# Kernel optimization log

Hardware: AMD Instinct MI355X
Metric: run time of the kernel (lower is better)

Reference implementation:

```python
import jax, jax.numpy as jnp
import numpy as np

B, CIN, H, W = 4, 1024, 64, 64
PLANES = 256
K = 3
DIL = 2
PAD = DIL * (K - 1) // 2  # = 2
EPS = 1e-5


def setup_inputs() -> dict:
    key = jax.random.key(0)
    ks = jax.random.split(key, 16)
    d = {}
    d['x'] = jax.random.normal(ks[0], (B, CIN, H, W), dtype=jnp.float32)
    # conv1: 1x1, inplanes->planes, no bias
    d['w1'] = jax.random.normal(ks[1], (PLANES, CIN), dtype=jnp.float32) * 0.02
    d['gamma1'] = jnp.ones((PLANES,), jnp.float32)
    d['beta1'] = jnp.zeros((PLANES,), jnp.float32)
    d['mean1'] = jax.random.normal(ks[2], (PLANES,), dtype=jnp.float32) * 0.1
    d['var1'] = jax.random.uniform(ks[3], (PLANES,), minval=0.5, maxval=1.5, dtype=jnp.float32)
    # deform_offset: 3x3 conv planes->18, with bias
    d['woff'] = jax.random.normal(ks[4], (18, PLANES, K, K), dtype=jnp.float32) * 0.01
    d['boff'] = jnp.zeros((18,), jnp.float32)
    # conv2 (deformable): 3x3 planes->planes, with bias
    d['w2'] = jax.random.normal(ks[5], (PLANES, PLANES, K, K), dtype=jnp.float32) * 0.02
    d['bconv2'] = jnp.zeros((PLANES,), jnp.float32)
    d['gamma2'] = jnp.ones((PLANES,), jnp.float32)
    d['beta2'] = jnp.zeros((PLANES,), jnp.float32)
    d['mean2'] = jax.random.normal(ks[6], (PLANES,), dtype=jnp.float32) * 0.1
    d['var2'] = jax.random.uniform(ks[7], (PLANES,), minval=0.5, maxval=1.5, dtype=jnp.float32)
    # conv3: 1x1 planes->planes*4, no bias
    d['w3'] = jax.random.normal(ks[8], (PLANES * 4, PLANES), dtype=jnp.float32) * 0.02
    d['gamma3'] = jnp.ones((PLANES * 4,), jnp.float32)
    d['beta3'] = jnp.zeros((PLANES * 4,), jnp.float32)
    d['mean3'] = jax.random.normal(ks[9], (PLANES * 4,), dtype=jnp.float32) * 0.1
    d['var3'] = jax.random.uniform(ks[10], (PLANES * 4,), minval=0.5, maxval=1.5, dtype=jnp.float32)
    return d


def _bn(x, gamma, beta, mean, var):
    # inference-mode BatchNorm over channel dim (NCHW)
    inv = jax.lax.rsqrt(var + EPS)
    return (x - mean[:, None, None]) * (inv * gamma)[:, None, None] + beta[:, None, None]


def _deform_conv(x, offset, w, b):
    # x: [B,C,H,W]; offset: [B,18,H,W] ordered (dy,dx) per kernel tap; w: [O,C,3,3]
    Bn, C, Hh, Ww = x.shape
    off = offset.reshape(Bn, K * K, 2, Hh, Ww)
    off_y, off_x = off[:, :, 0], off[:, :, 1]          # [B,9,H,W]
    kk = jnp.arange(K * K)
    base_y = (kk // K) * DIL - PAD                      # [9]
    base_x = (kk % K) * DIL - PAD
    ys = jnp.arange(Hh, dtype=x.dtype)
    xs = jnp.arange(Ww, dtype=x.dtype)
    py = base_y.astype(x.dtype)[None, :, None, None] + ys[None, None, :, None] + off_y
    px = base_x.astype(x.dtype)[None, :, None, None] + xs[None, None, None, :] + off_x

    def sample_one(img, py1, px1):
        # img [C,H,W]; py1/px1 [9,H,W] -> [C,9,H,W] bilinear with zero padding
        y0 = jnp.floor(py1)
        x0 = jnp.floor(px1)
        wy = py1 - y0
        wx = px1 - x0

        def gather(yc, xc):
            yi = yc.astype(jnp.int32)
            xi = xc.astype(jnp.int32)
            valid = ((yi >= 0) & (yi < Hh) & (xi >= 0) & (xi < Ww)).astype(img.dtype)
            yi = jnp.clip(yi, 0, Hh - 1)
            xi = jnp.clip(xi, 0, Ww - 1)
            return img[:, yi, xi] * valid[None]

        v00 = gather(y0, x0)
        v01 = gather(y0, x0 + 1)
        v10 = gather(y0 + 1, x0)
        v11 = gather(y0 + 1, x0 + 1)
        return (v00 * ((1 - wy) * (1 - wx))[None] + v01 * ((1 - wy) * wx)[None]
                + v10 * (wy * (1 - wx))[None] + v11 * (wy * wx)[None])

    sampled = jax.vmap(sample_one)(x, py, px)           # [B,C,9,H,W]
    out = jnp.einsum('bckhw,ock->bohw', sampled, w.reshape(w.shape[0], C, K * K))
    return out + b[None, :, None, None]


def reference(x, w1, gamma1, beta1, mean1, var1, woff, boff, w2, bconv2,
              gamma2, beta2, mean2, var2, w3, gamma3, beta3, mean3, var3):
    residual = x
    out = jnp.einsum('bchw,oc->bohw', x, w1)            # conv1 1x1
    out = jax.nn.relu(_bn(out, gamma1, beta1, mean1, var1))
    offset = jax.lax.conv_general_dilated(
        out, woff, window_strides=(1, 1), padding=((PAD, PAD), (PAD, PAD)),
        rhs_dilation=(DIL, DIL), dimension_numbers=('NCHW', 'OIHW', 'NCHW'))
    offset = offset + boff[None, :, None, None]
    out = _deform_conv(out, offset, w2, bconv2)
    out = jax.nn.relu(_bn(out, gamma2, beta2, mean2, var2))
    out = jnp.einsum('bchw,oc->bohw', out, w3)          # conv3 1x1
    out = _bn(out, gamma3, beta3, mean3, var3)
    return jax.nn.relu(out + residual)
```

## Files before the change

kernel.cpp:

```cpp
#include <hip/hip_runtime.h>

#define EPS_BN 1e-5f

typedef __bf16 bf16x8 __attribute__((ext_vector_type(8)));
typedef float f32x4 __attribute__((ext_vector_type(4)));

__device__ __forceinline__ unsigned short f2bf(float f) {
  union { float f; unsigned u; } v; v.f = f;
  unsigned r = v.u + 0x7fffu + ((v.u >> 16) & 1u);
  return (unsigned short)(r >> 16);
}
__device__ __forceinline__ float bf2f(unsigned short h) {
  union { unsigned u; float f; } v; v.u = ((unsigned)h) << 16;
  return v.f;
}

__global__ void cvt_bf16(const float* __restrict__ in, unsigned short* __restrict__ out, int n) {
  int i = blockIdx.x * 256 + threadIdx.x;
  if (i < n) out[i] = f2bf(in[i]);
}

__global__ void zero16(uint4* __restrict__ p, int n16) {
  int i = blockIdx.x * 256 + threadIdx.x;
  if (i < n16) p[i] = uint4{0, 0, 0, 0};
}

__global__ void reorder_w2(const float* __restrict__ w2, unsigned short* __restrict__ w2r) {
  int i = blockIdx.x * 256 + threadIdx.x;
  int o = i / 2304, r = i % 2304;
  int kk = r / 256, c = r % 256;
  w2r[i] = f2bf(w2[(size_t)o * 2304 + c * 9 + kk]);
}

__global__ void reorder_woff(const float* __restrict__ woff, unsigned short* __restrict__ wob) {
  int i = blockIdx.x * 256 + threadIdx.x;
  if (i >= 32 * 2304) return;
  int o = i / 2304, r = i % 2304;
  int kk = r / 256, c = r % 256;
  wob[i] = (o < 18) ? f2bf(woff[(size_t)o * 2304 + c * 9 + kk]) : (unsigned short)0;
}

__global__ __launch_bounds__(256) void transpose_x(const float* __restrict__ x,
                                                   unsigned short* __restrict__ xT) {
  __shared__ float t[32][33];
  int b = blockIdx.z;
  int p0 = blockIdx.x * 32, c0 = blockIdx.y * 32;
  int tx = threadIdx.x & 31, ty = threadIdx.x >> 5;
  const float* xb = x + (size_t)b * 1024 * 4096;
#pragma unroll
  for (int j = 0; j < 4; ++j) {
    int c = c0 + ty + j * 8;
    t[ty + j * 8][tx] = xb[(size_t)c * 4096 + p0 + tx];
  }
  __syncthreads();
  unsigned short* xTb = xT + (size_t)b * 4096 * 1024;
#pragma unroll
  for (int j = 0; j < 4; ++j) {
    int p = p0 + ty + j * 8;
    xTb[(size_t)p * 1024 + c0 + tx] = f2bf(t[tx][ty + j * 8]);
  }
}

template <int EPI>
__global__ __launch_bounds__(256) void gemm_bt(
    const unsigned short* __restrict__ A, const unsigned short* __restrict__ Bm,
    void* __restrict__ outp, unsigned short* __restrict__ out2,
    const float* __restrict__ gamma, const float* __restrict__ beta,
    const float* __restrict__ mean, const float* __restrict__ var,
    const float* __restrict__ bias, const float* __restrict__ resid,
    int M, int N, int K, long bStrideB, long bStrideOut) {
  __shared__ unsigned short sA[128 * 32];
  __shared__ unsigned short sB[128 * 32];
  int tid = threadIdx.x, lane = tid & 63, wv = tid >> 6;
  int z = blockIdx.z;
  const unsigned short* Bz = Bm + (size_t)z * bStrideB;
  int m0 = blockIdx.y * 128, n0 = blockIdx.x * 128;
  f32x4 acc[4][4] = {};
  int rowA = tid >> 2;
  int kcol = (tid & 3) * 8;
  int wm = wv & 1, wn = wv >> 1;
  int lane15 = lane & 15, quad8 = (lane >> 4) * 8;

  for (int k0 = 0; k0 < K; k0 += 32) {
    __syncthreads();
#pragma unroll
    for (int r = 0; r < 2; ++r) {
      const unsigned short* gp = A + (size_t)(m0 + r * 64 + rowA) * K + k0 + kcol;
      __builtin_amdgcn_global_load_lds((const __attribute__((address_space(1))) void*)gp,
                                       (__attribute__((address_space(3))) void*)&sA[r * 2048 + wv * 512],
                                       16, 0, 0);
    }
#pragma unroll
    for (int r = 0; r < 2; ++r) {
      const unsigned short* gp = Bz + (size_t)(n0 + r * 64 + rowA) * K + k0 + kcol;
      __builtin_amdgcn_global_load_lds((const __attribute__((address_space(1))) void*)gp,
                                       (__attribute__((address_space(3))) void*)&sB[r * 2048 + wv * 512],
                                       16, 0, 0);
    }
    __syncthreads();
    bf16x8 afr[4], bfr[4];
#pragma unroll
    for (int mi = 0; mi < 4; ++mi)
      afr[mi] = *(const bf16x8*)&sA[(wm * 64 + mi * 16 + lane15) * 32 + quad8];
#pragma unroll
    for (int ni = 0; ni < 4; ++ni)
      bfr[ni] = *(const bf16x8*)&sB[(wn * 64 + ni * 16 + lane15) * 32 + quad8];
#pragma unroll
    for (int mi = 0; mi < 4; ++mi)
#pragma unroll
      for (int ni = 0; ni < 4; ++ni)
        acc[mi][ni] = __builtin_amdgcn_mfma_f32_16x16x32_bf16(afr[mi], bfr[ni], acc[mi][ni], 0, 0, 0);
  }

  if constexpr (EPI == 3) {
    float* outF = (float*)outp + (size_t)z * bStrideOut;
    const float* res = resid + (size_t)z * bStrideOut;
#pragma unroll
    for (int mi = 0; mi < 4; ++mi) {
#pragma unroll
      for (int ni = 0; ni < 4; ++ni) {
        int col = n0 + wn * 64 + ni * 16 + lane15;
#pragma unroll
        for (int reg = 0; reg < 4; ++reg) {
          int row = m0 + wm * 64 + mi * 16 + (lane >> 4) * 4 + reg;
          int ch = row;
          float inv = rsqrtf(var[ch] + EPS_BN) * gamma[ch];
          float v = (acc[mi][ni][reg] - mean[ch]) * inv + beta[ch];
          v += res[(size_t)row * N + col];
          outF[(size_t)row * N + col] = fmaxf(v, 0.f);
        }
      }
    }
  } else {
    unsigned short* outH = (unsigned short*)outp;
#pragma unroll
    for (int mi = 0; mi < 4; ++mi) {
#pragma unroll
      for (int ni = 0; ni < 4; ++ni) {
        int col = n0 + wn * 64 + ni * 16 + lane15;
        int ch = col;
        float inv = rsqrtf(var[ch] + EPS_BN) * gamma[ch];
        float mu = mean[ch], bt = beta[ch];
        float bi = (EPI == 2) ? bias[ch] : 0.f;
#pragma unroll
        for (int reg = 0; reg < 4; ++reg) {
          int row = m0 + wm * 64 + mi * 16 + (lane >> 4) * 4 + reg;
          float v = acc[mi][ni][reg] + bi;
          v = (v - mu) * inv + bt;
          unsigned short hv = f2bf(fmaxf(v, 0.f));
          outH[(size_t)row * N + col] = hv;
          if constexpr (EPI == 1) {
            int b = row >> 12, p = row & 4095;
            out2[(((size_t)(b * 68) + (p >> 6) + 2) * 68 + (p & 63) + 2) * 256 + col] = hv;
          }
        }
      }
    }
  }
}

__global__ __launch_bounds__(256) void off_gemm(const unsigned short* __restrict__ actP,
                                                const unsigned short* __restrict__ wob,
                                                const float* __restrict__ boff,
                                                float* __restrict__ offsP) {
  __shared__ unsigned short sA[64 * 64];
  __shared__ unsigned short sB[32 * 64];
  int tid = threadIdx.x, lane = tid & 63, wv = tid >> 6;
  int m0 = blockIdx.x * 64;
  int lane15 = lane & 15, quad8 = (lane >> 4) * 8;
  int rowA = tid >> 3;
  int kc = (tid & 7) * 8;

  const unsigned short* baseA[2];
#pragma unroll
  for (int r = 0; r < 2; ++r) {
    int row = m0 + r * 32 + rowA;
    int b = row >> 12, p = row & 4095;
    baseA[r] = actP + (((size_t)(b * 68) + (p >> 6) + 2) * 68 + (p & 63) + 2) * 256 + kc;
  }
  const unsigned short* baseB = wob + (size_t)rowA * 2304 + kc;

  f32x4 acc[2] = {};
  for (int kk = 0; kk < 9; ++kk) {
    int shift = ((kk / 3) * 2 - 2) * 68 + ((kk % 3) * 2 - 2);
#pragma unroll 1
    for (int c0 = 0; c0 < 256; c0 += 64) {
      __syncthreads();
#pragma unroll
      for (int r = 0; r < 2; ++r) {
        const unsigned short* gp = baseA[r] + (long)shift * 256 + c0;
        __builtin_amdgcn_global_load_lds((const __attribute__((address_space(1))) void*)gp,
                                         (__attribute__((address_space(3))) void*)&sA[r * 2048 + wv * 512],
                                         16, 0, 0);
      }
      {
        const unsigned short* gp = baseB + kk * 256 + c0;
        __builtin_amdgcn_global_load_lds((const __attribute__((address_space(1))) void*)gp,
                                         (__attribute__((address_space(3))) void*)&sB[wv * 512],
                                         16, 0, 0);
      }
      __syncthreads();
      bf16x8 afr[2], bfr[2][2];
#pragma unroll
      for (int kq = 0; kq < 2; ++kq) {
        afr[kq] = *(const bf16x8*)&sA[(wv * 16 + lane15) * 64 + kq * 32 + quad8];
#pragma unroll
        for (int ni = 0; ni < 2; ++ni)
          bfr[kq][ni] = *(const bf16x8*)&sB[(ni * 16 + lane15) * 64 + kq * 32 + quad8];
      }
#pragma unroll
      for (int kq = 0; kq < 2; ++kq)
#pragma unroll
        for (int ni = 0; ni < 2; ++ni)
          acc[ni] = __builtin_amdgcn_mfma_f32_16x16x32_bf16(afr[kq], bfr[kq][ni], acc[ni], 0, 0, 0);
    }
  }

#pragma unroll
  for (int ni = 0; ni < 2; ++ni) {
    int o = ni * 16 + lane15;
    if (o < 18) {
      float bo = boff[o];
#pragma unroll
      for (int reg = 0; reg < 4; ++reg) {
        int row = m0 + wv * 16 + (lane >> 4) * 4 + reg;
        offsP[(size_t)row * 18 + o] = acc[ni][reg] + bo;
      }
    }
  }
}

__global__ __launch_bounds__(256) void deform_sample(const unsigned short* __restrict__ act1T,
                                                     const float* __restrict__ offsP,
                                                     unsigned short* __restrict__ S) {
  int g = threadIdx.x >> 5, t = threadIdx.x & 31;
  int idx = blockIdx.x * 8 + g;
  int b = idx >> 12, p = idx & 4095;
  int h = p >> 6, w = p & 63;
  const unsigned short* actb = act1T + (size_t)b * 4096 * 256 + t * 8;
  unsigned short* Sp = S + (size_t)idx * 2304 + t * 8;
  float ov = (t < 18) ? offsP[(size_t)idx * 18 + t] : 0.f;
#pragma unroll
  for (int kk = 0; kk < 9; ++kk) {
    float offy = __shfl(ov, 2 * kk, 32);
    float offx = __shfl(ov, 2 * kk + 1, 32);
    float py = (float)(h + (kk / 3) * 2 - 2) + offy;
    float px = (float)(w + (kk % 3) * 2 - 2) + offx;
    float fy = floorf(py), fx = floorf(px);
    int y0 = (int)fy, x0 = (int)fx;
    float wy = py - fy, wx = px - fx;
    bool yv0 = (y0 >= 0 && y0 < 64), yv1 = (y0 >= -1 && y0 < 63);
    bool xv0 = (x0 >= 0 && x0 < 64), xv1 = (x0 >= -1 && x0 < 63);
    const unsigned short* cb = actb + (y0 * 64 + x0) * 256;
    uint4 q00{0,0,0,0}, q01{0,0,0,0}, q10{0,0,0,0}, q11{0,0,0,0};
    if (yv0 && xv0) q00 = *(const uint4*)(cb);
    if (yv0 && xv1) q01 = *(const uint4*)(cb + 256);
    if (yv1 && xv0) q10 = *(const uint4*)(cb + 64 * 256);
    if (yv1 && xv1) q11 = *(const uint4*)(cb + 64 * 256 + 256);
    float w00 = (1.f - wy) * (1.f - wx), w01 = (1.f - wy) * wx;
    float w10 = wy * (1.f - wx), w11 = wy * wx;
    unsigned u00[4] = {q00.x, q00.y, q00.z, q00.w};
    unsigned u01[4] = {q01.x, q01.y, q01.z, q01.w};
    unsigned u10[4] = {q10.x, q10.y, q10.z, q10.w};
    unsigned u11[4] = {q11.x, q11.y, q11.z, q11.w};
    unsigned out[4];
#pragma unroll
    for (int j = 0; j < 4; ++j) {
      float lo = bf2f((unsigned short)(u00[j] & 0xffffu)) * w00 +
                 bf2f((unsigned short)(u01[j] & 0xffffu)) * w01 +
                 bf2f((unsigned short)(u10[j] & 0xffffu)) * w10 +
                 bf2f((unsigned short)(u11[j] & 0xffffu)) * w11;
      float hi = bf2f((unsigned short)(u00[j] >> 16)) * w00 +
                 bf2f((unsigned short)(u01[j] >> 16)) * w01 +
                 bf2f((unsigned short)(u10[j] >> 16)) * w10 +
                 bf2f((unsigned short)(u11[j] >> 16)) * w11;
      out[j] = (unsigned)f2bf(lo) | ((unsigned)f2bf(hi) << 16);
    }
    *(uint4*)(Sp + kk * 256) = uint4{out[0], out[1], out[2], out[3]};
  }
}

extern "C" void kernel_launch(void* const* d_in, const int* in_sizes, int n_in,
                              void* d_out, int out_size, void* d_ws, size_t ws_size,
                              hipStream_t stream) {
  const float* x      = (const float*)d_in[0];
  const float* w1     = (const float*)d_in[1];
  const float* gamma1 = (const float*)d_in[2];
  const float* beta1  = (const float*)d_in[3];
  const float* mean1  = (const float*)d_in[4];
  const float* var1   = (const float*)d_in[5];
  const float* woff   = (const float*)d_in[6];
  const float* boff   = (const float*)d_in[7];
  const float* w2     = (const float*)d_in[8];
  const float* bconv2 = (const float*)d_in[9];
  const float* gamma2 = (const float*)d_in[10];
  const float* beta2  = (const float*)d_in[11];
  const float* mean2  = (const float*)d_in[12];
  const float* var2   = (const float*)d_in[13];
  const float* w3     = (const float*)d_in[14];
  const float* gamma3 = (const float*)d_in[15];
  const float* beta3  = (const float*)d_in[16];
  const float* mean3  = (const float*)d_in[17];
  const float* var3   = (const float*)d_in[18];

  char* ws = (char*)d_ws;
  unsigned short* xT    = (unsigned short*)(ws);
  unsigned short* act1T = (unsigned short*)(ws + 33554432);
  unsigned short* act2T = (unsigned short*)(ws + 41943040);
  unsigned short* S     = (unsigned short*)(ws + 50331648);
  float*          offs  = (float*)(ws + 125829120);
  unsigned short* w1b   = (unsigned short*)(ws + 127008768);
  unsigned short* w2r   = (unsigned short*)(ws + 127533056);
  unsigned short* w3b   = (unsigned short*)(ws + 128712704);
  unsigned short* act1P = S;
  unsigned short* wob   = xT;

  cvt_bf16<<<1024, 256, 0, stream>>>(w1, w1b, 262144);
  cvt_bf16<<<1024, 256, 0, stream>>>(w3, w3b, 262144);
  reorder_w2<<<2304, 256, 0, stream>>>(w2, w2r);
  zero16<<<2312, 256, 0, stream>>>((uint4*)act1P, 591872);
  transpose_x<<<dim3(128, 32, 4), 256, 0, stream>>>(x, xT);

  gemm_bt<1><<<dim3(2, 128, 1), 256, 0, stream>>>(xT, w1b, act1T, act1P, gamma1, beta1, mean1,
                                                  var1, nullptr, nullptr, 16384, 256, 1024, 0, 0);
  reorder_woff<<<288, 256, 0, stream>>>(woff, wob);
  off_gemm<<<256, 256, 0, stream>>>(act1P, wob, boff, offs);
  deform_sample<<<dim3(2048), 256, 0, stream>>>(act1T, offs, S);
  gemm_bt<2><<<dim3(2, 128, 1), 256, 0, stream>>>(S, w2r, act2T, nullptr, gamma2, beta2, mean2,
                                                  var2, bconv2, nullptr, 16384, 256, 2304, 0, 0);
  gemm_bt<3><<<dim3(32, 8, 4), 256, 0, stream>>>(w3b, act2T, d_out, nullptr, gamma3, beta3, mean3,
                                                 var3, nullptr, x, 1024, 4096, 256, 4096L * 256,
                                                 4194304L);
}
```

Baseline: 325.9 us.

## Split-K the conv1 and deformable GEMMs with a separate vectorized BN epilogue

The two M=16384,N=256 GEMMs ran only 256 blocks each. They now use split-K by two (512 blocks), writing fp32 partials that a new vectorized epilogue kernel sums before applying precomputed BN scale and shift, ReLU and bf16 packing, including the padded copy. This adds fp32 partial-sum traffic of about 32MB written and read per GEMM, plus extra launches. In exchange it gets more parallelism and coalesced 16-byte epilogue stores in place of scattered 2-byte stores.

```diff
diff --git a/kernel.cpp b/kernel.cpp
--- a/kernel.cpp
+++ b/kernel.cpp
@@ -38,6 +38,16 @@
   int o = i / 2304, r = i % 2304;
   int kk = r / 256, c = r % 256;
   wob[i] = (o < 18) ? f2bf(woff[(size_t)o * 2304 + c * 9 + kk]) : (unsigned short)0;
+}
+
+__global__ void prep_bn(const float* g1, const float* b1, const float* m1, const float* v1,
+                        const float* g2, const float* b2, const float* m2, const float* v2,
+                        const float* bconv2, float* s1, float* h1, float* s2, float* h2) {
+  int c = threadIdx.x;
+  float sc1 = rsqrtf(v1[c] + EPS_BN) * g1[c];
+  s1[c] = sc1; h1[c] = b1[c] - m1[c] * sc1;
+  float sc2 = rsqrtf(v2[c] + EPS_BN) * g2[c];
+  s2[c] = sc2; h2[c] = b2[c] + (bconv2[c] - m2[c]) * sc2;
 }
 
 __global__ __launch_bounds__(256) void transpose_x(const float* __restrict__ x,
@@ -61,14 +71,102 @@
   }
 }
 
-template <int EPI>
-__global__ __launch_bounds__(256) void gemm_bt(
+__global__ __launch_bounds__(256) void gemm_split(
     const unsigned short* __restrict__ A, const unsigned short* __restrict__ Bm,
-    void* __restrict__ outp, unsigned short* __restrict__ out2,
-    const float* __restrict__ gamma, const float* __restrict__ beta,
+    float* __restrict__ part, int M, int N, int K, int KH) {
+  __shared__ unsigned short sA[128 * 32];
+  __shared__ unsigned short sB[128 * 32];
+  int tid = threadIdx.x, lane = tid & 63, wv = tid >> 6;
+  int z = blockIdx.z;
+  int m0 = blockIdx.y * 128, n0 = blockIdx.x * 128;
+  f32x4 acc[4][4] = {};
+  int rowA = tid >> 2;
+  int kcol = (tid & 3) * 8;
+  int wm = wv & 1, wn = wv >> 1;
+  int lane15 = lane & 15, quad8 = (lane >> 4) * 8;
+  int kend = z * KH + KH;
+
+  for (int k0 = z * KH; k0 < kend; k0 += 32) {
+    __syncthreads();
+#pragma unroll
+    for (int r = 0; r < 2; ++r) {
+      const unsigned short* gp = A + (size_t)(m0 + r * 64 + rowA) * K + k0 + kcol;
+      __builtin_amdgcn_global_load_lds((const __attribute__((address_space(1))) void*)gp,
+                                       (__attribute__((address_space(3))) void*)&sA[r * 2048 + wv * 512],
+                                       16, 0, 0);
+    }
+#pragma unroll
+    for (int r = 0; r < 2; ++r) {
+      const unsigned short* gp = Bm + (size_t)(n0 + r * 64 + rowA) * K + k0 + kcol;
+      __builtin_amdgcn_global_load_lds((const __attribute__((address_space(1))) void*)gp,
+                                       (__attribute__((address_space(3))) void*)&sB[r * 2048 + wv * 512],
+                                       16, 0, 0);
+    }
+    __syncthreads();
+    bf16x8 afr[4], bfr[4];
+#pragma unroll
+    for (int mi = 0; mi < 4; ++mi)
+      afr[mi] = *(const bf16x8*)&sA[(wm * 64 + mi * 16 + lane15) * 32 + quad8];
+#pragma unroll
+    for (int ni = 0; ni < 4; ++ni)
+      bfr[ni] = *(const bf16x8*)&sB[(wn * 64 + ni * 16 + lane15) * 32 + quad8];
+#pragma unroll
+    for (int mi = 0; mi < 4; ++mi)
+#pragma unroll
+      for (int ni = 0; ni < 4; ++ni)
+        acc[mi][ni] = __builtin_amdgcn_mfma_f32_16x16x32_bf16(afr[mi], bfr[ni], acc[mi][ni], 0, 0, 0);
+  }
+
+  float* outF = part + (size_t)z * M * N;
+#pragma unroll
+  for (int mi = 0; mi < 4; ++mi) {
+#pragma unroll
+    for (int ni = 0; ni < 4; ++ni) {
+      int col = n0 + wn * 64 + ni * 16 + lane15;
+#pragma unroll
+      for (int reg = 0; reg < 4; ++reg) {
+        int row = m0 + wm * 64 + mi * 16 + (lane >> 4) * 4 + reg;
+        outF[(size_t)row * N + col] = acc[mi][ni][reg];
+      }
+    }
+  }
+}
+
+template <int PAD>
+__global__ __launch_bounds__(256) void epi_bn(const float* __restrict__ part,
+                                              const float* __restrict__ scale,
+                                              const float* __restrict__ shift,
+                                              unsigned short* __restrict__ outT,
+                                              unsigned short* __restrict__ outP) {
+  int gid = blockIdx.x * 256 + threadIdx.x;
+  int row = gid >> 5, c0 = (gid & 31) * 8;
+  const float* a = part + (size_t)row * 256 + c0;
+  const float* b = a + (size_t)16384 * 256;
+  float va[8], vb[8], sc[8], sh[8];
+  *(float4*)&va[0] = *(const float4*)a;       *(float4*)&va[4] = *(const float4*)(a + 4);
+  *(float4*)&vb[0] = *(const float4*)b;       *(float4*)&vb[4] = *(const float4*)(b + 4);
+  *(float4*)&sc[0] = *(const float4*)(scale + c0); *(float4*)&sc[4] = *(const float4*)(scale + c0 + 4);
+  *(float4*)&sh[0] = *(const float4*)(shift + c0); *(float4*)&sh[4] = *(const float4*)(shift + c0 + 4);
+  unsigned o[4];
+#pragma unroll
+  for (int j = 0; j < 4; ++j) {
+    float lo = fmaxf((va[2 * j] + vb[2 * j]) * sc[2 * j] + sh[2 * j], 0.f);
+    float hi = fmaxf((va[2 * j + 1] + vb[2 * j + 1]) * sc[2 * j + 1] + sh[2 * j + 1], 0.f);
+    o[j] = (unsigned)f2bf(lo) | ((unsigned)f2bf(hi) << 16);
+  }
+  uint4 pk{o[0], o[1], o[2], o[3]};
+  *(uint4*)(outT + (size_t)row * 256 + c0) = pk;
+  if constexpr (PAD) {
+    int bb = row >> 12, p = row & 4095;
+    *(uint4*)(outP + (((size_t)(bb * 68) + (p >> 6) + 2) * 68 + (p & 63) + 2) * 256 + c0) = pk;
+  }
+}
+
+__global__ __launch_bounds__(256) void gemm_res(
+    const unsigned short* __restrict__ A, const unsigned short* __restrict__ Bm,
+    float* __restrict__ outp, const float* __restrict__ gamma, const float* __restrict__ beta,
     const float* __restrict__ mean, const float* __restrict__ var,
-    const float* __restrict__ bias, const float* __restrict__ resid,
-    int M, int N, int K, long bStrideB, long bStrideOut) {
+    const float* __restrict__ resid, int M, int N, int K, long bStrideB, long bStrideOut) {
   __shared__ unsigned short sA[128 * 32];
   __shared__ unsigned short sB[128 * 32];
   int tid = threadIdx.x, lane = tid & 63, wv = tid >> 6;
@@ -112,48 +210,21 @@
         acc[mi][ni] = __builtin_amdgcn_mfma_f32_16x16x32_bf16(afr[mi], bfr[ni], acc[mi][ni], 0, 0, 0);
   }
 
-  if constexpr (EPI == 3) {
-    float* outF = (float*)outp + (size_t)z * bStrideOut;
-    const float* res = resid + (size_t)z * bStrideOut;
-#pragma unroll
-    for (int mi = 0; mi < 4; ++mi) {
-#pragma unroll
-      for (int ni = 0; ni < 4; ++ni) {
-        int col = n0 + wn * 64 + ni * 16 + lane15;
-#pragma unroll
-        for (int reg = 0; reg < 4; ++reg) {
-          int row = m0 + wm * 64 + mi * 16 + (lane >> 4) * 4 + reg;
-          int ch = row;
-          float inv = rsqrtf(var[ch] + EPS_BN) * gamma[ch];
-          float v = (acc[mi][ni][reg] - mean[ch]) * inv + beta[ch];
-          v += res[(size_t)row * N + col];
-          outF[(size_t)row * N + col] = fmaxf(v, 0.f);
-        }
-      }
-    }
-  } else {
-    unsigned short* outH = (unsigned short*)outp;
-#pragma unroll
-    for (int mi = 0; mi < 4; ++mi) {
-#pragma unroll
-      for (int ni = 0; ni < 4; ++ni) {
-        int col = n0 + wn * 64 + ni * 16 + lane15;
-        int ch = col;
+  float* outF = outp + (size_t)z * bStrideOut;
+  const float* res = resid + (size_t)z * bStrideOut;
+#pragma unroll
+  for (int mi = 0; mi < 4; ++mi) {
+#pragma unroll
+    for (int ni = 0; ni < 4; ++ni) {
+      int col = n0 + wn * 64 + ni * 16 + lane15;
+#pragma unroll
+      for (int reg = 0; reg < 4; ++reg) {
+        int row = m0 + wm * 64 + mi * 16 + (lane >> 4) * 4 + reg;
+        int ch = row;
         float inv = rsqrtf(var[ch] + EPS_BN) * gamma[ch];
-        float mu = mean[ch], bt = beta[ch];
-        float bi = (EPI == 2) ? bias[ch] : 0.f;
-#pragma unroll
-        for (int reg = 0; reg < 4; ++reg) {
-          int row = m0 + wm * 64 + mi * 16 + (lane >> 4) * 4 + reg;
-          float v = acc[mi][ni][reg] + bi;
-          v = (v - mu) * inv + bt;
-          unsigned short hv = f2bf(fmaxf(v, 0.f));
-          outH[(size_t)row * N + col] = hv;
-          if constexpr (EPI == 1) {
-            int b = row >> 12, p = row & 4095;
-            out2[(((size_t)(b * 68) + (p >> 6) + 2) * 68 + (p & 63) + 2) * 256 + col] = hv;
-          }
-        }
+        float v = (acc[mi][ni][reg] - mean[ch]) * inv + beta[ch];
+        v += res[(size_t)row * N + col];
+        outF[(size_t)row * N + col] = fmaxf(v, 0.f);
       }
     }
   }
@@ -312,23 +383,33 @@
   unsigned short* w1b   = (unsigned short*)(ws + 127008768);
   unsigned short* w2r   = (unsigned short*)(ws + 127533056);
   unsigned short* w3b   = (unsigned short*)(ws + 128712704);
+  float*          bnS1  = (float*)(ws + 129236992);
+  float*          bnH1  = (float*)(ws + 129238016);
+  float*          bnS2  = (float*)(ws + 129239040);
+  float*          bnH2  = (float*)(ws + 129240064);
   unsigned short* act1P = S;
+  float*          part1 = (float*)(ws + 62914560);
+  float*          part2 = (float*)ws;
   unsigned short* wob   = xT;
 
   cvt_bf16<<<1024, 256, 0, stream>>>(w1, w1b, 262144);
   cvt_bf16<<<1024, 256, 0, stream>>>(w3, w3b, 262144);
   reorder_w2<<<2304, 256, 0, stream>>>(w2, w2r);
   zero16<<<2312, 256, 0, stream>>>((uint4*)act1P, 591872);
+  prep_bn<<<1, 256, 0, stream>>>(gamma1, beta1, mean1, var1, gamma2, beta2, mean2, var2,
+                                 bconv2, bnS1, bnH1, bnS2, bnH2);
   transpose_x<<<dim3(128, 32, 4), 256, 0, stream>>>(x, xT);
 
-  gemm_bt<1><<<dim3(2, 128, 1), 256, 0, stream>>>(xT, w1b, act1T, act1P, gamma1, beta1, mean1,
-                                                  var1, nullptr, nullptr, 16384, 256, 1024, 0, 0);
+  gemm_split<<<dim3(2, 128, 2), 256, 0, stream>>>(xT, w1b, part1, 16384, 256, 1024, 512);
+  epi_bn<1><<<2048, 256, 0, stream>>>(part1, bnS1, bnH1, act1T, act1P);
+
   reorder_woff<<<288, 256, 0, stream>>>(woff, wob);
   off_gemm<<<256, 256, 0, stream>>>(act1P, wob, boff, offs);
   deform_sample<<<dim3(2048), 256, 0, stream>>>(act1T, offs, S);
-  gemm_bt<2><<<dim3(2, 128, 1), 256, 0, stream>>>(S, w2r, act2T, nullptr, gamma2, beta2, mean2,
-                                                  var2, bconv2, nullptr, 16384, 256, 2304, 0, 0);
-  gemm_bt<3><<<dim3(32, 8, 4), 256, 0, stream>>>(w3b, act2T, d_out, nullptr, gamma3, beta3, mean3,
-                                                 var3, nullptr, x, 1024, 4096, 256, 4096L * 256,
-                                                 4194304L);
-}
+
+  gemm_split<<<dim3(2, 128, 2), 256, 0, stream>>>(S, w2r, part2, 16384, 256, 2304, 1152);
+  epi_bn<0><<<2048, 256, 0, stream>>>(part2, bnS2, bnH2, act2T, nullptr);
+
+  gemm_res<<<dim3(32, 8, 4), 256, 0, stream>>>(w3b, act2T, (float*)d_out, gamma3, beta3, mean3,
+                                               var3, x, 1024, 4096, 256, 4096L * 256, 4194304L);
+}
```

Result: no change. 322.4 us (-1.1%).
